# Performance work log

Hardware: AMD Instinct MI355X
Metric: run time of the kernel (lower is better)

## Reference

```python
import jax, jax.numpy as jnp
import numpy as np

N_HEAD = 16
N_KV_HEAD = 4
HEAD_DIM = 64  # n_embd // n_head = 1024 // 16
N_EMBD = 1024


def _alibi_bias(T, n_head, head_dim):
    # slopes: start = 2**(-2**(-(log2(H)-3))); slope_i = start**(i+1)
    start = 2.0 ** (-2.0 ** (-(np.log2(n_head) - 3.0)))
    slopes = jnp.asarray(start ** np.arange(1, n_head + 1), dtype=jnp.float32)  # [H]
    rel = (jnp.arange(T, dtype=jnp.float32)[None, :]
           - jnp.arange(T, dtype=jnp.float32)[:, None])  # [T,T], rel[i,j] = j - i
    bias = slopes[:, None, None] * rel[None, :, :]  # [H,T,T]
    # Faithful to the torch module: masked_fill(-inf) is then OVERWRITTEN by
    # torch.tril, which zeroes the upper triangle. Net effect: lower-tri alibi
    # values, 0 above the diagonal (NO causal masking).
    bias = jnp.tril(bias)
    return bias * (head_dim ** -0.5)  # extra scale applied in forward


def setup_inputs() -> dict:
    key = jax.random.key(0)
    ks = jax.random.split(key, 5)
    B, T, C = 4, 2048, N_EMBD
    w_scale = 0.02
    return {
        "x": jax.random.normal(ks[0], (B, T, C), dtype=jnp.float32),
        "Wq": jax.random.normal(ks[1], (C, C), dtype=jnp.float32) * w_scale,
        "Wkv": jax.random.normal(ks[2], (2 * N_KV_HEAD * HEAD_DIM, C), dtype=jnp.float32) * w_scale,
        "Wproj": jax.random.normal(ks[3], (C, C), dtype=jnp.float32) * w_scale,
        "bproj": jnp.zeros((C,), dtype=jnp.float32),
    }


def reference(x, Wq, Wkv, Wproj, bproj):
    B, T, C = x.shape
    H, KVH, D = N_HEAD, N_KV_HEAD, HEAD_DIM
    ratio = H // KVH

    q = jnp.einsum('btc,ec->bte', x, Wq).reshape(B, T, H, D).transpose(0, 2, 1, 3)  # [B,H,T,D]
    kv = jnp.einsum('btc,ec->bte', x, Wkv)  # [B,T,2*KVH*D]
    k, v = jnp.split(kv, 2, axis=-1)
    k = k.reshape(B, T, KVH, D).transpose(0, 2, 1, 3)  # [B,KVH,T,D]
    v = v.reshape(B, T, KVH, D).transpose(0, 2, 1, 3)
    # torch .repeat tiles whole blocks: query head h uses kv head h % KVH
    k = jnp.tile(k, (1, ratio, 1, 1))  # [B,H,T,D]
    v = jnp.tile(v, (1, ratio, 1, 1))

    bias = _alibi_bias(T, H, D)  # [H,T,T], already *= D**-0.5
    scores = jnp.einsum('bhtd,bhsd->bhts', q, k) * (D ** -0.5) + bias[None]
    attn = jax.nn.softmax(scores, axis=-1)
    out = jnp.einsum('bhts,bhsd->bhtd', attn, v)  # [B,H,T,D]
    out = out.transpose(0, 2, 1, 3).reshape(B, T, C)
    return jnp.einsum('btc,ec->bte', out, Wproj) + bproj
```

## Files before the change

kernel.cpp:

```cpp
#include <hip/hip_runtime.h>
#include <hip/hip_bf16.h>
#include <cstdint>

typedef __bf16 bf16;
typedef bf16 bf16x2 __attribute__((ext_vector_type(2)));
typedef bf16 bf16x4 __attribute__((ext_vector_type(4)));
typedef bf16 bf16x8 __attribute__((ext_vector_type(8)));
typedef float f32x4 __attribute__((ext_vector_type(4)));

#define MFMA16(a, b, c) __builtin_amdgcn_mfma_f32_16x16x32_bf16((a), (b), (c), 0, 0, 0)

#define QSCALE 0.18033688011112042f

__device__ inline void async16(const bf16* g, bf16* l) {
  __builtin_amdgcn_global_load_lds(
      (const __attribute__((address_space(1))) void*)g,
      (__attribute__((address_space(3))) void*)l, 16, 0, 0);
}

__global__ void cast_all(const float* __restrict__ x, const float* __restrict__ wq,
                         const float* __restrict__ wkv, const float* __restrict__ wp,
                         bf16* __restrict__ xb, bf16* __restrict__ w1b,
                         bf16* __restrict__ wpb) {
  const int i = blockIdx.x * blockDim.x + threadIdx.x;
  const float4* src;
  bf16x4* dst;
  int idx;
  if (i < 2097152) {
    src = (const float4*)x; dst = (bf16x4*)xb; idx = i;
  } else if (i < 2359296) {
    src = (const float4*)wq; dst = (bf16x4*)w1b; idx = i - 2097152;
  } else if (i < 2490368) {
    src = (const float4*)wkv; dst = (bf16x4*)(w1b + 1048576); idx = i - 2359296;
  } else {
    src = (const float4*)wp; dst = (bf16x4*)wpb; idx = i - 2490368;
  }
  const float4 v = src[idx];
  bf16x4 o;
  o.x = (bf16)v.x; o.y = (bf16)v.y; o.z = (bf16)v.z; o.w = (bf16)v.w;
  dst[idx] = o;
}

__global__ __launch_bounds__(256, 2)
void gemm_qkv(const bf16* __restrict__ A, const bf16* __restrict__ B,
              bf16* __restrict__ qb, bf16* __restrict__ kb, bf16* __restrict__ vb) {
  constexpr int K = 1024;
  __shared__ bf16 sA[128 * 64];
  __shared__ bf16 sB[128 * 64];
  const int tid = threadIdx.x;
  const int lane = tid & 63, wid = tid >> 6;
  const int col = lane & 15, quad = lane >> 4;
  const int wm = wid >> 1, wn = wid & 1;
  const int m0 = blockIdx.y * 128, n0 = blockIdx.x * 128;
  const int c7 = col & 7;

  f32x4 acc[4][4];
  const f32x4 z = {0.f, 0.f, 0.f, 0.f};
#pragma unroll
  for (int mi = 0; mi < 4; mi++)
#pragma unroll
    for (int ni = 0; ni < 4; ni++) acc[mi][ni] = z;

  for (int k0 = 0; k0 < K; k0 += 64) {
    __syncthreads();
#pragma unroll
    for (int c = 0; c < 4; ++c) {
      const int idx = c * 256 + tid;
      const int row = idx >> 3, kc = idx & 7;
      const int gkc = kc ^ (row & 7);
      async16(&A[(size_t)(m0 + row) * K + k0 + gkc * 8], &sA[idx * 8]);
      async16(&B[(size_t)(n0 + row) * K + k0 + gkc * 8], &sB[idx * 8]);
    }
    __syncthreads();
#pragma unroll
    for (int ks = 0; ks < 2; ++ks) {
      bf16x8 af[4], bfr[4];
#pragma unroll
      for (int i = 0; i < 4; i++)
        af[i] = *(const bf16x8*)&sA[(wm * 64 + i * 16 + col) * 64 +
                                    (((ks * 4 + quad) ^ c7) << 3)];
#pragma unroll
      for (int i = 0; i < 4; i++)
        bfr[i] = *(const bf16x8*)&sB[(wn * 64 + i * 16 + col) * 64 +
                                     (((ks * 4 + quad) ^ c7) << 3)];
#pragma unroll
      for (int mi = 0; mi < 4; mi++)
#pragma unroll
        for (int ni = 0; ni < 4; ni++)
          acc[mi][ni] = MFMA16(af[mi], bfr[ni], acc[mi][ni]);
    }
  }
#pragma unroll
  for (int mi = 0; mi < 4; mi++) {
#pragma unroll
    for (int ni = 0; ni < 4; ni++) {
      const int e = n0 + wn * 64 + ni * 16 + col;
#pragma unroll
      for (int r = 0; r < 4; r++) {
        const int m = m0 + wm * 64 + mi * 16 + quad * 4 + r;
        const int bb = m >> 11, t = m & 2047;
        if (e < 1024) {
          qb[(((size_t)bb * 16 + (e >> 6)) * 2048 + t) * 64 + (e & 63)] =
              (bf16)(acc[mi][ni][r] * QSCALE);
        } else if (e < 1280) {
          const int f = e - 1024;
          kb[(((size_t)bb * 4 + (f >> 6)) * 2048 + t) * 64 + (f & 63)] =
              (bf16)acc[mi][ni][r];
        } else {
          const int f = e - 1280;
          vb[(((size_t)bb * 4 + (f >> 6)) * 2048 + t) * 64 + (f & 63)] =
              (bf16)acc[mi][ni][r];
        }
      }
    }
  }
}

__global__ __launch_bounds__(256, 2)
void gemm_proj(const bf16* __restrict__ A, const bf16* __restrict__ B,
               const float* __restrict__ bias, float* __restrict__ out) {
  constexpr int K = 1024;
  __shared__ bf16 sA[128 * 64];
  __shared__ bf16 sB[128 * 64];
  const int tid = threadIdx.x;
  const int lane = tid & 63, wid = tid >> 6;
  const int col = lane & 15, quad = lane >> 4;
  const int wm = wid >> 1, wn = wid & 1;
  const int m0 = blockIdx.y * 128, n0 = blockIdx.x * 128;
  const int c7 = col & 7;

  f32x4 acc[4][4];
  const f32x4 z = {0.f, 0.f, 0.f, 0.f};
#pragma unroll
  for (int mi = 0; mi < 4; mi++)
#pragma unroll
    for (int ni = 0; ni < 4; ni++) acc[mi][ni] = z;

  for (int k0 = 0; k0 < K; k0 += 64) {
    __syncthreads();
#pragma unroll
    for (int c = 0; c < 4; ++c) {
      const int idx = c * 256 + tid;
      const int row = idx >> 3, kc = idx & 7;
      const int gkc = kc ^ (row & 7);
      async16(&A[(size_t)(m0 + row) * K + k0 + gkc * 8], &sA[idx * 8]);
      async16(&B[(size_t)(n0 + row) * K + k0 + gkc * 8], &sB[idx * 8]);
    }
    __syncthreads();
#pragma unroll
    for (int ks = 0; ks < 2; ++ks) {
      bf16x8 af[4], bfr[4];
#pragma unroll
      for (int i = 0; i < 4; i++)
        af[i] = *(const bf16x8*)&sA[(wm * 64 + i * 16 + col) * 64 +
                                    (((ks * 4 + quad) ^ c7) << 3)];
#pragma unroll
      for (int i = 0; i < 4; i++)
        bfr[i] = *(const bf16x8*)&sB[(wn * 64 + i * 16 + col) * 64 +
                                     (((ks * 4 + quad) ^ c7) << 3)];
#pragma unroll
      for (int mi = 0; mi < 4; mi++)
#pragma unroll
        for (int ni = 0; ni < 4; ni++)
          acc[mi][ni] = MFMA16(af[mi], bfr[ni], acc[mi][ni]);
    }
  }
#pragma unroll
  for (int mi = 0; mi < 4; mi++) {
#pragma unroll
    for (int ni = 0; ni < 4; ni++) {
      const int e = n0 + wn * 64 + ni * 16 + col;
      const float be = bias[e];
#pragma unroll
      for (int r = 0; r < 4; r++) {
        const int m = m0 + wm * 64 + mi * 16 + quad * 4 + r;
        out[(size_t)m * 1024 + e] = acc[mi][ni][r] + be;
      }
    }
  }
}

__global__ __launch_bounds__(256, 2)
void attn_alibi(const bf16* __restrict__ qb, const bf16* __restrict__ kb,
                const bf16* __restrict__ vb, bf16* __restrict__ ob) {
  __shared__ bf16 sK[2][64 * 64];
  __shared__ bf16 sVt[2][64 * 72];
  __shared__ bf16 sPt[4][64 * 64];
  const int tid = threadIdx.x;
  const int lane = tid & 63, wid = tid >> 6;
  const int col = lane & 15, quad = lane >> 4;
  const int c7 = col & 7;
  const int bh = blockIdx.y;
  const int b = bh >> 4, h = bh & 15, kvh = h & 3;
  const int qbase = __builtin_amdgcn_readfirstlane(blockIdx.x * 256 + wid * 64);

  const bf16* qptr = qb + ((size_t)(b * 16 + h) * 2048 + qbase) * 64;
  const bf16* kptr = kb + ((size_t)(b * 4 + kvh) * 2048) * 64;
  const bf16* vptr = vb + ((size_t)(b * 4 + kvh) * 2048) * 64;

  bf16x8 bq[4][2];
#pragma unroll
  for (int ni = 0; ni < 4; ni++)
#pragma unroll
    for (int ks = 0; ks < 2; ks++)
      bq[ni][ks] = *(const bf16x8*)&qptr[(ni * 16 + col) * 64 + ks * 32 + quad * 8];

  bf16x8 bones;
#pragma unroll
  for (int j = 0; j < 8; j++) bones[j] = (bf16)1.0f;

  f32x4 O[4][4];
  f32x4 Osum[4];
  const f32x4 z = {0.f, 0.f, 0.f, 0.f};
#pragma unroll
  for (int mi = 0; mi < 4; mi++) {
    Osum[mi] = z;
#pragma unroll
    for (int nd = 0; nd < 4; nd++) O[mi][nd] = z;
  }

  const float cb = exp2f(-0.5f * (float)(h + 1)) * QSCALE;
  const int qoff = quad * 4 - col;

  const int rk0 = tid >> 3, rk1 = 32 + rk0, kc = tid & 7;
  const int rv = rk0 * 2;
  const int blkv = rv >> 3, rlv = rv & 7;
  const int kx = (kc ^ (rk0 & 7)) << 3;

  bf16x8 kr0 = *(const bf16x8*)&kptr[(size_t)rk0 * 64 + kc * 8];
  bf16x8 kr1 = *(const bf16x8*)&kptr[(size_t)rk1 * 64 + kc * 8];
  bf16x8 vr0 = *(const bf16x8*)&vptr[(size_t)rv * 64 + kc * 8];
  bf16x8 vr1 = *(const bf16x8*)&vptr[(size_t)(rv + 1) * 64 + kc * 8];

  int bufi = 0;
  for (int c0 = 0; c0 < 2048; c0 += 64, bufi ^= 1) {
    bf16* skw = sK[bufi];
    bf16* svw = sVt[bufi];
    *(bf16x8*)&skw[rk0 * 64 + kx] = kr0;
    *(bf16x8*)&skw[rk1 * 64 + kx] = kr1;
#pragma unroll
    for (int j = 0; j < 8; j++) {
      bf16x2 pr;
      pr.x = vr0[j];
      pr.y = vr1[j];
      *(bf16x2*)&svw[(kc * 8 + j) * 72 + ((blkv ^ kc) << 3) + rlv] = pr;
    }
    __syncthreads();

    {
      const int cn = (c0 + 64 < 2048) ? c0 + 64 : 0;
      kr0 = *(const bf16x8*)&kptr[(size_t)(cn + rk0) * 64 + kc * 8];
      kr1 = *(const bf16x8*)&kptr[(size_t)(cn + rk1) * 64 + kc * 8];
      vr0 = *(const bf16x8*)&vptr[(size_t)(cn + rv) * 64 + kc * 8];
      vr1 = *(const bf16x8*)&vptr[(size_t)(cn + rv + 1) * 64 + kc * 8];
    }

    f32x4 S[4][4];
#pragma unroll
    for (int mi = 0; mi < 4; mi++)
#pragma unroll
      for (int ni = 0; ni < 4; ni++) S[mi][ni] = z;
#pragma unroll
    for (int ks = 0; ks < 2; ks++) {
      bf16x8 ak[4];
#pragma unroll
      for (int mi = 0; mi < 4; mi++)
        ak[mi] = *(const bf16x8*)&skw[(mi * 16 + col) * 64 +
                                      (((ks * 4 + quad) ^ c7) << 3)];
#pragma unroll
      for (int mi = 0; mi < 4; mi++)
#pragma unroll
        for (int ni = 0; ni < 4; ni++)
          S[mi][ni] = MFMA16(ak[mi], bq[ni][ks], S[mi][ni]);
    }

    bf16* sp = sPt[wid];
#pragma unroll
    for (int ni = 0; ni < 4; ni++) {
#pragma unroll
      for (int mi = 0; mi < 4; mi++) {
        const int U = c0 + mi * 16 - qbase - ni * 16;
        f32x4 p;
        if (U <= -15) {
          const float bb = cb * (float)(U + qoff);
#pragma unroll
          for (int r = 0; r < 4; r++)
            p[r] = __builtin_amdgcn_exp2f(S[mi][ni][r] + (bb + cb * (float)r));
        } else if (U >= 16) {
#pragma unroll
          for (int r = 0; r < 4; r++)
            p[r] = __builtin_amdgcn_exp2f(S[mi][ni][r]);
        } else {
          const float relf = (float)(U + qoff);
#pragma unroll
          for (int r = 0; r < 4; r++) {
            const float rr = relf + (float)r;
            const float bb = (rr <= 0.f) ? cb * rr : 0.f;
            p[r] = __builtin_amdgcn_exp2f(S[mi][ni][r] + bb);
          }
        }
        bf16x4 w;
#pragma unroll
        for (int r = 0; r < 4; r++) w[r] = (bf16)p[r];
        *(bf16x4*)&sp[(ni * 16 + col) * 64 +
                      (((2 * mi + (quad >> 1)) ^ c7) << 3) + ((quad & 1) << 2)] = w;
      }
    }

#pragma unroll
    for (int ks = 0; ks < 2; ks++) {
      bf16x8 ap[4], bv[4];
#pragma unroll
      for (int mi = 0; mi < 4; mi++)
        ap[mi] = *(const bf16x8*)&sp[(mi * 16 + col) * 64 +
                                     (((ks * 4 + quad) ^ c7) << 3)];
#pragma unroll
      for (int nd = 0; nd < 4; nd++) {
        const int d = nd * 16 + col;
        bv[nd] = *(const bf16x8*)&svw[d * 72 + (((ks * 4 + quad) ^ (d >> 3)) << 3)];
      }
#pragma unroll
      for (int mi = 0; mi < 4; mi++) {
#pragma unroll
        for (int nd = 0; nd < 4; nd++)
          O[mi][nd] = MFMA16(ap[mi], bv[nd], O[mi][nd]);
        Osum[mi] = MFMA16(ap[mi], bones, Osum[mi]);
      }
    }
  }

#pragma unroll
  for (int mi = 0; mi < 4; mi++) {
#pragma unroll
    for (int r = 0; r < 4; r++) {
      const float inv = 1.0f / Osum[mi][r];
      const int t = qbase + mi * 16 + quad * 4 + r;
#pragma unroll
      for (int nd = 0; nd < 4; nd++) {
        ob[((size_t)b * 2048 + t) * 1024 + h * 64 + nd * 16 + col] =
            (bf16)(O[mi][nd][r] * inv);
      }
    }
  }
}

extern "C" void kernel_launch(void* const* d_in, const int* in_sizes, int n_in,
                              void* d_out, int out_size, void* d_ws, size_t ws_size,
                              hipStream_t stream) {
  const float* x     = (const float*)d_in[0];
  const float* Wq    = (const float*)d_in[1];
  const float* Wkv   = (const float*)d_in[2];
  const float* Wproj = (const float*)d_in[3];
  const float* bproj = (const float*)d_in[4];
  float* out = (float*)d_out;

  bf16* xb  = (bf16*)d_ws;
  bf16* w1b = xb  + 8388608;
  bf16* wpb = w1b + 1572864;
  bf16* qb  = wpb + 1048576;
  bf16* kb  = qb  + 8388608;
  bf16* vb  = kb  + 2097152;
  bf16* aob = vb  + 2097152;

  cast_all<<<10752, 256, 0, stream>>>(x, Wq, Wkv, Wproj, xb, w1b, wpb);
  gemm_qkv<<<dim3(12, 64), 256, 0, stream>>>(xb, w1b, qb, kb, vb);
  attn_alibi<<<dim3(8, 64), 256, 0, stream>>>(qb, kb, vb, aob);
  gemm_proj<<<dim3(8, 64), 256, 0, stream>>>(aob, wpb, bproj, out);
}
```

Measured before the change: 240.4 us.

## Keep P in registers via transposed PV MFMA with fp16 V, load K directly

The attention kernel now computes O transposed so the probability tile produced by the QK^T MFMA can feed the PV MFMA (16x16x16 f16) straight from registers, removing the per-wave P shared-memory round trip. K fragments are loaded from global memory straight into registers with a one-tile register prefetch, dropping the K shared-memory buffer. V is stored as fp16 by the QKV GEMM so probabilities can be converted to f16. This adds register pressure and uses a smaller-K MFMA with more instructions, and it changes the precision of V and P.

```diff
diff --git a/kernel.cpp b/kernel.cpp
--- a/kernel.cpp
+++ b/kernel.cpp
@@ -6,9 +6,14 @@
 typedef bf16 bf16x2 __attribute__((ext_vector_type(2)));
 typedef bf16 bf16x4 __attribute__((ext_vector_type(4)));
 typedef bf16 bf16x8 __attribute__((ext_vector_type(8)));
+typedef _Float16 f16;
+typedef f16 f16x2 __attribute__((ext_vector_type(2)));
+typedef f16 f16x4 __attribute__((ext_vector_type(4)));
+typedef f16 f16x8 __attribute__((ext_vector_type(8)));
 typedef float f32x4 __attribute__((ext_vector_type(4)));
 
 #define MFMA16(a, b, c) __builtin_amdgcn_mfma_f32_16x16x32_bf16((a), (b), (c), 0, 0, 0)
+#define MFMA16H(a, b, c) __builtin_amdgcn_mfma_f32_16x16x16f16((a), (b), (c), 0, 0, 0)
 
 #define QSCALE 0.18033688011112042f
 
@@ -43,7 +48,7 @@
 
 __global__ __launch_bounds__(256, 2)
 void gemm_qkv(const bf16* __restrict__ A, const bf16* __restrict__ B,
-              bf16* __restrict__ qb, bf16* __restrict__ kb, bf16* __restrict__ vb) {
+              bf16* __restrict__ qb, bf16* __restrict__ kb, f16* __restrict__ vb) {
   constexpr int K = 1024;
   __shared__ bf16 sA[128 * 64];
   __shared__ bf16 sB[128 * 64];
@@ -109,7 +114,7 @@
         } else {
           const int f = e - 1280;
           vb[(((size_t)bb * 4 + (f >> 6)) * 2048 + t) * 64 + (f & 63)] =
-              (bf16)acc[mi][ni][r];
+              (f16)acc[mi][ni][r];
         }
       }
     }
@@ -181,22 +186,19 @@
 }
 
 __global__ __launch_bounds__(256, 2)
-void attn_alibi(const bf16* __restrict__ qb, const bf16* __restrict__ kb,
-                const bf16* __restrict__ vb, bf16* __restrict__ ob) {
-  __shared__ bf16 sK[2][64 * 64];
-  __shared__ bf16 sVt[2][64 * 72];
-  __shared__ bf16 sPt[4][64 * 64];
+void attn_alibi(const bf16* __restrict__ qb, const bf16* __restrict__ kbp,
+                const f16* __restrict__ vbp, bf16* __restrict__ ob) {
+  __shared__ f16 sVt[2][64 * 72];
   const int tid = threadIdx.x;
   const int lane = tid & 63, wid = tid >> 6;
   const int col = lane & 15, quad = lane >> 4;
-  const int c7 = col & 7;
   const int bh = blockIdx.y;
   const int b = bh >> 4, h = bh & 15, kvh = h & 3;
   const int qbase = __builtin_amdgcn_readfirstlane(blockIdx.x * 256 + wid * 64);
 
   const bf16* qptr = qb + ((size_t)(b * 16 + h) * 2048 + qbase) * 64;
-  const bf16* kptr = kb + ((size_t)(b * 4 + kvh) * 2048) * 64;
-  const bf16* vptr = vb + ((size_t)(b * 4 + kvh) * 2048) * 64;
+  const bf16* kptr = kbp + ((size_t)(b * 4 + kvh) * 2048) * 64;
+  const f16* vptr = vbp + ((size_t)(b * 4 + kvh) * 2048) * 64;
 
   bf16x8 bq[4][2];
 #pragma unroll
@@ -205,141 +207,129 @@
     for (int ks = 0; ks < 2; ks++)
       bq[ni][ks] = *(const bf16x8*)&qptr[(ni * 16 + col) * 64 + ks * 32 + quad * 8];
 
-  bf16x8 bones;
-#pragma unroll
-  for (int j = 0; j < 8; j++) bones[j] = (bf16)1.0f;
-
-  f32x4 O[4][4];
-  f32x4 Osum[4];
+  f16x4 ones;
+#pragma unroll
+  for (int j = 0; j < 4; j++) ones[j] = (f16)1.0f;
+
+  f32x4 OT[4][4];
+  f32x4 lC[4];
   const f32x4 z = {0.f, 0.f, 0.f, 0.f};
 #pragma unroll
-  for (int mi = 0; mi < 4; mi++) {
-    Osum[mi] = z;
-#pragma unroll
-    for (int nd = 0; nd < 4; nd++) O[mi][nd] = z;
+  for (int nd = 0; nd < 4; nd++) {
+    lC[nd] = z;
+#pragma unroll
+    for (int ni = 0; ni < 4; ni++) OT[nd][ni] = z;
   }
 
   const float cb = exp2f(-0.5f * (float)(h + 1)) * QSCALE;
   const int qoff = quad * 4 - col;
 
-  const int rk0 = tid >> 3, rk1 = 32 + rk0, kc = tid & 7;
-  const int rv = rk0 * 2;
-  const int blkv = rv >> 3, rlv = rv & 7;
-  const int kx = (kc ^ (rk0 & 7)) << 3;
-
-  bf16x8 kr0 = *(const bf16x8*)&kptr[(size_t)rk0 * 64 + kc * 8];
-  bf16x8 kr1 = *(const bf16x8*)&kptr[(size_t)rk1 * 64 + kc * 8];
-  bf16x8 vr0 = *(const bf16x8*)&vptr[(size_t)rv * 64 + kc * 8];
-  bf16x8 vr1 = *(const bf16x8*)&vptr[(size_t)(rv + 1) * 64 + kc * 8];
+  bf16x8 ak[4][2];
+#pragma unroll
+  for (int mi = 0; mi < 4; mi++)
+#pragma unroll
+    for (int ks = 0; ks < 2; ks++)
+      ak[mi][ks] = *(const bf16x8*)&kptr[(size_t)(mi * 16 + col) * 64 + ks * 32 + quad * 8];
+
+  const int pv = tid & 31, kcv = tid >> 5;
+  f16x8 vr0 = *(const f16x8*)&vptr[(size_t)(2 * pv) * 64 + kcv * 8];
+  f16x8 vr1 = *(const f16x8*)&vptr[(size_t)(2 * pv + 1) * 64 + kcv * 8];
 
   int bufi = 0;
   for (int c0 = 0; c0 < 2048; c0 += 64, bufi ^= 1) {
-    bf16* skw = sK[bufi];
-    bf16* svw = sVt[bufi];
-    *(bf16x8*)&skw[rk0 * 64 + kx] = kr0;
-    *(bf16x8*)&skw[rk1 * 64 + kx] = kr1;
+    f16* sv = sVt[bufi];
 #pragma unroll
     for (int j = 0; j < 8; j++) {
-      bf16x2 pr;
+      f16x2 pr;
       pr.x = vr0[j];
       pr.y = vr1[j];
-      *(bf16x2*)&svw[(kc * 8 + j) * 72 + ((blkv ^ kc) << 3) + rlv] = pr;
-    }
-    __syncthreads();
-
-    {
-      const int cn = (c0 + 64 < 2048) ? c0 + 64 : 0;
-      kr0 = *(const bf16x8*)&kptr[(size_t)(cn + rk0) * 64 + kc * 8];
-      kr1 = *(const bf16x8*)&kptr[(size_t)(cn + rk1) * 64 + kc * 8];
-      vr0 = *(const bf16x8*)&vptr[(size_t)(cn + rv) * 64 + kc * 8];
-      vr1 = *(const bf16x8*)&vptr[(size_t)(cn + rv + 1) * 64 + kc * 8];
-    }
+      *(f16x2*)&sv[(kcv * 8 + j) * 72 + 2 * pv] = pr;
+    }
+    __syncthreads();
+
+    const int cn = (c0 + 64 < 2048) ? c0 + 64 : 0;
+    bf16x8 akn[4][2];
+#pragma unroll
+    for (int mi = 0; mi < 4; mi++)
+#pragma unroll
+      for (int ks = 0; ks < 2; ks++)
+        akn[mi][ks] = *(const bf16x8*)&kptr[(size_t)(cn + mi * 16 + col) * 64 +
+                                            ks * 32 + quad * 8];
+    f16x8 vr0n = *(const f16x8*)&vptr[(size_t)(cn + 2 * pv) * 64 + kcv * 8];
+    f16x8 vr1n = *(const f16x8*)&vptr[(size_t)(cn + 2 * pv + 1) * 64 + kcv * 8];
 
     f32x4 S[4][4];
 #pragma unroll
-    for (int mi = 0; mi < 4; mi++)
-#pragma unroll
-      for (int ni = 0; ni < 4; ni++) S[mi][ni] = z;
-#pragma unroll
-    for (int ks = 0; ks < 2; ks++) {
-      bf16x8 ak[4];
-#pragma unroll
-      for (int mi = 0; mi < 4; mi++)
-        ak[mi] = *(const bf16x8*)&skw[(mi * 16 + col) * 64 +
-                                      (((ks * 4 + quad) ^ c7) << 3)];
-#pragma unroll
-      for (int mi = 0; mi < 4; mi++)
+    for (int kb = 0; kb < 4; kb++)
+#pragma unroll
+      for (int ni = 0; ni < 4; ni++) S[kb][ni] = z;
+#pragma unroll
+    for (int ks = 0; ks < 2; ks++)
+#pragma unroll
+      for (int kb = 0; kb < 4; kb++)
 #pragma unroll
         for (int ni = 0; ni < 4; ni++)
-          S[mi][ni] = MFMA16(ak[mi], bq[ni][ks], S[mi][ni]);
-    }
-
-    bf16* sp = sPt[wid];
-#pragma unroll
-    for (int ni = 0; ni < 4; ni++) {
-#pragma unroll
-      for (int mi = 0; mi < 4; mi++) {
-        const int U = c0 + mi * 16 - qbase - ni * 16;
+          S[kb][ni] = MFMA16(ak[kb][ks], bq[ni][ks], S[kb][ni]);
+
+#pragma unroll
+    for (int kb = 0; kb < 4; kb++) {
+      f16x4 pf[4];
+#pragma unroll
+      for (int ni = 0; ni < 4; ni++) {
+        const int U = c0 + kb * 16 - qbase - ni * 16;
         f32x4 p;
         if (U <= -15) {
           const float bb = cb * (float)(U + qoff);
 #pragma unroll
           for (int r = 0; r < 4; r++)
-            p[r] = __builtin_amdgcn_exp2f(S[mi][ni][r] + (bb + cb * (float)r));
+            p[r] = __builtin_amdgcn_exp2f(S[kb][ni][r] + (bb + cb * (float)r));
         } else if (U >= 16) {
 #pragma unroll
           for (int r = 0; r < 4; r++)
-            p[r] = __builtin_amdgcn_exp2f(S[mi][ni][r]);
+            p[r] = __builtin_amdgcn_exp2f(S[kb][ni][r]);
         } else {
           const float relf = (float)(U + qoff);
 #pragma unroll
           for (int r = 0; r < 4; r++) {
             const float rr = relf + (float)r;
             const float bb = (rr <= 0.f) ? cb * rr : 0.f;
-            p[r] = __builtin_amdgcn_exp2f(S[mi][ni][r] + bb);
+            p[r] = __builtin_amdgcn_exp2f(S[kb][ni][r] + bb);
           }
         }
-        bf16x4 w;
-#pragma unroll
-        for (int r = 0; r < 4; r++) w[r] = (bf16)p[r];
-        *(bf16x4*)&sp[(ni * 16 + col) * 64 +
-                      (((2 * mi + (quad >> 1)) ^ c7) << 3) + ((quad & 1) << 2)] = w;
+#pragma unroll
+        for (int r = 0; r < 4; r++) pf[ni][r] = (f16)p[r];
       }
-    }
-
-#pragma unroll
-    for (int ks = 0; ks < 2; ks++) {
-      bf16x8 ap[4], bv[4];
-#pragma unroll
-      for (int mi = 0; mi < 4; mi++)
-        ap[mi] = *(const bf16x8*)&sp[(mi * 16 + col) * 64 +
-                                     (((ks * 4 + quad) ^ c7) << 3)];
-#pragma unroll
-      for (int nd = 0; nd < 4; nd++) {
-        const int d = nd * 16 + col;
-        bv[nd] = *(const bf16x8*)&svw[d * 72 + (((ks * 4 + quad) ^ (d >> 3)) << 3)];
+      f16x4 av[4];
+#pragma unroll
+      for (int nd = 0; nd < 4; nd++)
+        av[nd] = *(const f16x4*)&sv[(nd * 16 + col) * 72 + kb * 16 + quad * 4];
+#pragma unroll
+      for (int ni = 0; ni < 4; ni++) {
+#pragma unroll
+        for (int nd = 0; nd < 4; nd++)
+          OT[nd][ni] = MFMA16H(av[nd], pf[ni], OT[nd][ni]);
+        lC[ni] = MFMA16H(ones, pf[ni], lC[ni]);
       }
-#pragma unroll
-      for (int mi = 0; mi < 4; mi++) {
-#pragma unroll
-        for (int nd = 0; nd < 4; nd++)
-          O[mi][nd] = MFMA16(ap[mi], bv[nd], O[mi][nd]);
-        Osum[mi] = MFMA16(ap[mi], bones, Osum[mi]);
-      }
-    }
-  }
-
-#pragma unroll
-  for (int mi = 0; mi < 4; mi++) {
-#pragma unroll
-    for (int r = 0; r < 4; r++) {
-      const float inv = 1.0f / Osum[mi][r];
-      const int t = qbase + mi * 16 + quad * 4 + r;
-#pragma unroll
-      for (int nd = 0; nd < 4; nd++) {
-        ob[((size_t)b * 2048 + t) * 1024 + h * 64 + nd * 16 + col] =
-            (bf16)(O[mi][nd][r] * inv);
-      }
+    }
+
+#pragma unroll
+    for (int mi = 0; mi < 4; mi++)
+#pragma unroll
+      for (int ks = 0; ks < 2; ks++) ak[mi][ks] = akn[mi][ks];
+    vr0 = vr0n;
+    vr1 = vr1n;
+  }
+
+#pragma unroll
+  for (int ni = 0; ni < 4; ni++) {
+    const float inv = 1.0f / lC[ni][0];
+    const size_t rowb = ((size_t)b * 2048 + qbase + ni * 16 + col) * 1024 + h * 64;
+#pragma unroll
+    for (int nd = 0; nd < 4; nd++) {
+      bf16x4 w;
+#pragma unroll
+      for (int r = 0; r < 4; r++) w[r] = (bf16)(OT[nd][ni][r] * inv);
+      *(bf16x4*)&ob[rowb + nd * 16 + quad * 4] = w;
     }
   }
 }
@@ -359,8 +349,8 @@
   bf16* wpb = w1b + 1572864;
   bf16* qb  = wpb + 1048576;
   bf16* kb  = qb  + 8388608;
-  bf16* vb  = kb  + 2097152;
-  bf16* aob = vb  + 2097152;
+  f16*  vb  = (f16*)(kb + 2097152);
+  bf16* aob = (bf16*)(vb + 2097152);
 
   cast_all<<<10752, 256, 0, stream>>>(x, Wq, Wkv, Wproj, xb, w1b, wpb);
   gemm_qkv<<<dim3(12, 64), 256, 0, stream>>>(xb, w1b, qb, kb, vb);
```

Measured after the change: 259.2 us. 7.8% more time.

## Single-buffer K/V LDS tiles and interleave softmax exp with PV MFMAs

Applied to the files above, without the earlier changes.

Replaces the double-buffered K and V^T shared-memory tiles with a single buffer, adding a barrier at the top of each iteration so the old tile is consumed before it is overwritten. This cuts LDS usage, which could allow more resident blocks. The exp/bf16 conversion of P is split by key half (ks), so each half's PV MFMAs can start right after that half is written, overlapping transcendental work with matrix ops. The cost is an extra __syncthreads per iteration.

```diff
diff --git a/kernel.cpp b/kernel.cpp
--- a/kernel.cpp
+++ b/kernel.cpp
@@ -181,10 +181,10 @@
 }
 
 __global__ __launch_bounds__(256, 2)
-void attn_alibi(const bf16* __restrict__ qb, const bf16* __restrict__ kb,
-                const bf16* __restrict__ vb, bf16* __restrict__ ob) {
-  __shared__ bf16 sK[2][64 * 64];
-  __shared__ bf16 sVt[2][64 * 72];
+void attn_alibi(const bf16* __restrict__ qb, const bf16* __restrict__ kbp,
+                const bf16* __restrict__ vbp, bf16* __restrict__ ob) {
+  __shared__ bf16 sK[64 * 64];
+  __shared__ bf16 sVt[64 * 72];
   __shared__ bf16 sPt[4][64 * 64];
   const int tid = threadIdx.x;
   const int lane = tid & 63, wid = tid >> 6;
@@ -195,8 +195,8 @@
   const int qbase = __builtin_amdgcn_readfirstlane(blockIdx.x * 256 + wid * 64);
 
   const bf16* qptr = qb + ((size_t)(b * 16 + h) * 2048 + qbase) * 64;
-  const bf16* kptr = kb + ((size_t)(b * 4 + kvh) * 2048) * 64;
-  const bf16* vptr = vb + ((size_t)(b * 4 + kvh) * 2048) * 64;
+  const bf16* kptr = kbp + ((size_t)(b * 4 + kvh) * 2048) * 64;
+  const bf16* vptr = vbp + ((size_t)(b * 4 + kvh) * 2048) * 64;
 
   bf16x8 bq[4][2];
 #pragma unroll
@@ -232,18 +232,18 @@
   bf16x8 vr0 = *(const bf16x8*)&vptr[(size_t)rv * 64 + kc * 8];
   bf16x8 vr1 = *(const bf16x8*)&vptr[(size_t)(rv + 1) * 64 + kc * 8];
 
-  int bufi = 0;
-  for (int c0 = 0; c0 < 2048; c0 += 64, bufi ^= 1) {
-    bf16* skw = sK[bufi];
-    bf16* svw = sVt[bufi];
-    *(bf16x8*)&skw[rk0 * 64 + kx] = kr0;
-    *(bf16x8*)&skw[rk1 * 64 + kx] = kr1;
+  bf16* sp = sPt[wid];
+
+  for (int c0 = 0; c0 < 2048; c0 += 64) {
+    __syncthreads();
+    *(bf16x8*)&sK[rk0 * 64 + kx] = kr0;
+    *(bf16x8*)&sK[rk1 * 64 + kx] = kr1;
 #pragma unroll
     for (int j = 0; j < 8; j++) {
       bf16x2 pr;
       pr.x = vr0[j];
       pr.y = vr1[j];
-      *(bf16x2*)&svw[(kc * 8 + j) * 72 + ((blkv ^ kc) << 3) + rlv] = pr;
+      *(bf16x2*)&sVt[(kc * 8 + j) * 72 + ((blkv ^ kc) << 3) + rlv] = pr;
     }
     __syncthreads();
 
@@ -265,8 +265,8 @@
       bf16x8 ak[4];
 #pragma unroll
       for (int mi = 0; mi < 4; mi++)
-        ak[mi] = *(const bf16x8*)&skw[(mi * 16 + col) * 64 +
-                                      (((ks * 4 + quad) ^ c7) << 3)];
+        ak[mi] = *(const bf16x8*)&sK[(mi * 16 + col) * 64 +
+                                     (((ks * 4 + quad) ^ c7) << 3)];
 #pragma unroll
       for (int mi = 0; mi < 4; mi++)
 #pragma unroll
@@ -274,41 +274,41 @@
           S[mi][ni] = MFMA16(ak[mi], bq[ni][ks], S[mi][ni]);
     }
 
-    bf16* sp = sPt[wid];
-#pragma unroll
-    for (int ni = 0; ni < 4; ni++) {
-#pragma unroll
-      for (int mi = 0; mi < 4; mi++) {
-        const int U = c0 + mi * 16 - qbase - ni * 16;
-        f32x4 p;
-        if (U <= -15) {
-          const float bb = cb * (float)(U + qoff);
-#pragma unroll
-          for (int r = 0; r < 4; r++)
-            p[r] = __builtin_amdgcn_exp2f(S[mi][ni][r] + (bb + cb * (float)r));
-        } else if (U >= 16) {
-#pragma unroll
-          for (int r = 0; r < 4; r++)
-            p[r] = __builtin_amdgcn_exp2f(S[mi][ni][r]);
-        } else {
-          const float relf = (float)(U + qoff);
-#pragma unroll
-          for (int r = 0; r < 4; r++) {
-            const float rr = relf + (float)r;
-            const float bb = (rr <= 0.f) ? cb * rr : 0.f;
-            p[r] = __builtin_amdgcn_exp2f(S[mi][ni][r] + bb);
+#pragma unroll
+    for (int ks = 0; ks < 2; ks++) {
+#pragma unroll
+      for (int mh = 0; mh < 2; mh++) {
+        const int mi = ks * 2 + mh;
+#pragma unroll
+        for (int ni = 0; ni < 4; ni++) {
+          const int U = c0 + mi * 16 - qbase - ni * 16;
+          f32x4 p;
+          if (U <= -15) {
+            const float bb = cb * (float)(U + qoff);
+#pragma unroll
+            for (int r = 0; r < 4; r++)
+              p[r] = __builtin_amdgcn_exp2f(S[mi][ni][r] + (bb + cb * (float)r));
+          } else if (U >= 16) {
+#pragma unroll
+            for (int r = 0; r < 4; r++)
+              p[r] = __builtin_amdgcn_exp2f(S[mi][ni][r]);
+          } else {
+            const float relf = (float)(U + qoff);
+#pragma unroll
+            for (int r = 0; r < 4; r++) {
+              const float rr = relf + (float)r;
+              const float bb = (rr <= 0.f) ? cb * rr : 0.f;
+              p[r] = __builtin_amdgcn_exp2f(S[mi][ni][r] + bb);
+            }
           }
+          bf16x4 w;
+#pragma unroll
+          for (int r = 0; r < 4; r++) w[r] = (bf16)p[r];
+          *(bf16x4*)&sp[(ni * 16 + col) * 64 +
+                        (((2 * mi + (quad >> 1)) ^ c7) << 3) + ((quad & 1) << 2)] = w;
         }
-        bf16x4 w;
-#pragma unroll
-        for (int r = 0; r < 4; r++) w[r] = (bf16)p[r];
-        *(bf16x4*)&sp[(ni * 16 + col) * 64 +
-                      (((2 * mi + (quad >> 1)) ^ c7) << 3) + ((quad & 1) << 2)] = w;
-      }
-    }
-
-#pragma unroll
-    for (int ks = 0; ks < 2; ks++) {
+      }
+
       bf16x8 ap[4], bv[4];
 #pragma unroll
       for (int mi = 0; mi < 4; mi++)
@@ -317,7 +317,7 @@
 #pragma unroll
       for (int nd = 0; nd < 4; nd++) {
         const int d = nd * 16 + col;
-        bv[nd] = *(const bf16x8*)&svw[d * 72 + (((ks * 4 + quad) ^ (d >> 3)) << 3)];
+        bv[nd] = *(const bf16x8*)&sVt[d * 72 + (((ks * 4 + quad) ^ (d >> 3)) << 3)];
       }
 #pragma unroll
       for (int mi = 0; mi < 4; mi++) {
```

New measurement: 254.0 us. 1.06x slower.
